# Optimization experiments

Hardware: AMD Instinct MI355X
Metric: run time of the kernel (lower is better)

The kernel has to match this reference:

```python
import jax, jax.numpy as jnp
import numpy as np

B, C_IN, C_MID, C_OUT, H, W = 256, 2, 128, 64, 15, 15
N_RES = 4  # line_length//2 - 1 with line_length=11

# per-direction input offsets for kernel taps w0 and w2 (w1 is always center),
# matching fix_direction_order=True sparse 3x3 kernel construction:
# dir0 horizontal, dir1 vertical, dir2 anti-diagonal, dir3 main diagonal.
OFFSETS = (((0, -1), (0, 1)),
           ((-1, 0), (1, 0)),
           ((1, -1), (-1, 1)),
           ((-1, -1), (1, 1)))


def shift2d(x, di, dj):
    # out[..., i, j] = x[..., i+di, j+dj] with zero padding (di,dj in {-1,0,1})
    nd = x.ndim
    xp = jnp.pad(x, [(0, 0)] * (nd - 2) + [(1, 1), (1, 1)])
    h, w = x.shape[-2], x.shape[-1]
    return xp[..., 1 + di:1 + di + h, 1 + dj:1 + dj + w]


def dir_conv(x, w, b):
    # x: [4,B,Cin,H,W]; w: [Cout,Cin,3]; b: [Cout]
    x0 = jnp.stack([shift2d(x[d], *OFFSETS[d][0]) for d in range(4)])
    x2 = jnp.stack([shift2d(x[d], *OFFSETS[d][1]) for d in range(4)])
    y = (jnp.einsum('oc,dbchw->dbohw', w[..., 0], x0)
         + jnp.einsum('oc,dbchw->dbohw', w[..., 1], x)
         + jnp.einsum('oc,dbchw->dbohw', w[..., 2], x2))
    return y + b[None, None, :, None, None]


def conv1x1(x, w, b):
    # x: [4,B,Cin,H,W]; w: [Cout,Cin]; b: [Cout]
    return jnp.einsum('oc,dbchw->dbohw', w, x) + b[None, None, :, None, None]


def setup_inputs() -> dict:
    key = jax.random.key(0)
    ks = jax.random.split(key, 16)
    s_in = 1.0 / np.sqrt(3 * C_IN)
    s_mid = 1.0 / np.sqrt(3 * C_MID)
    s_pw = 1.0 / np.sqrt(C_MID)
    return {
        'x': jax.random.normal(ks[0], (B, C_IN, H, W), jnp.float32),
        'dconv0_w': jax.random.normal(ks[1], (C_MID, C_IN, 3), jnp.float32) * s_in,
        'dconv0_b': jnp.zeros((C_MID,), jnp.float32),
        'res_dconv_w': jax.random.normal(ks[2], (N_RES, C_MID, C_MID, 3), jnp.float32) * s_mid,
        'res_dconv_b': jnp.zeros((N_RES, C_MID), jnp.float32),
        'res_pw_w': jax.random.normal(ks[3], (N_RES, C_MID, C_MID), jnp.float32) * s_pw,
        'res_pw_b': jnp.zeros((N_RES, C_MID), jnp.float32),
        'c0_w1': jax.random.normal(ks[4], (C_MID, C_MID), jnp.float32) * s_pw,
        'c0_b1': jnp.zeros((C_MID,), jnp.float32),
        'c0_w2': jax.random.normal(ks[5], (C_MID, C_MID), jnp.float32) * s_pw,
        'c0_b2': jnp.zeros((C_MID,), jnp.float32),
        'final_w': jax.random.normal(ks[6], (C_OUT, C_MID), jnp.float32) * s_pw,
        'final_b': jnp.zeros((C_OUT,), jnp.float32),
    }


def reference(x, dconv0_w, dconv0_b, res_dconv_w, res_dconv_b,
              res_pw_w, res_pw_b, c0_w1, c0_b1, c0_w2, c0_b2,
              final_w, final_b):
    act = jax.nn.silu
    # all 4 direction streams start from the same input plane
    h = jnp.broadcast_to(x[None], (4,) + x.shape)  # [4,B,Cin,H,W]
    h = act(dir_conv(h, dconv0_w, dconv0_b))
    # DirectionalConvResBlocks (norm='none')
    for i in range(N_RES):
        r = h
        h = act(dir_conv(h, res_dconv_w[i], res_dconv_b[i]))
        h = act(conv1x1(h, res_pw_w[i], res_pw_b[i]))
        h = h + r
    # Conv0dResBlock (two 1x1 convs, middle_dim_multipler=1)
    r = h
    h = act(conv1x1(h, c0_w1, c0_b1))
    h = act(conv1x1(h, c0_w2, c0_b2))
    h = h + r
    # final 1x1 conv, then stack directions at dim=1 -> [B,4,Cout,H,W]
    h = conv1x1(h, final_w, final_b)
    return jnp.transpose(h, (1, 0, 2, 3, 4))
```

## Files before the change

kernel.cpp:

```cpp
#include <hip/hip_runtime.h>

using u16 = unsigned short;
using u32 = unsigned int;

typedef __bf16 bf16x8 __attribute__((ext_vector_type(8)));
typedef float  f32x4  __attribute__((ext_vector_type(4)));

#define NPOS   225
#define NT     15
#define ROWP   136
#define A_ROWS 289
#define B_ROWS 241
#define A_ELEMS (A_ROWS*ROWP)
#define B_ELEMS (B_ROWS*ROWP)
#define LDS_BYTES ((A_ELEMS + B_ELEMS)*2)
#define RSTRIDE17 (17*ROWP)

#define WA_PER_L 49152
#define WP_OFF   (4*WA_PER_L)
#define WP_PER   16384
#define WF_OFF   (WP_OFF + 6*WP_PER)
#define W_U16_TOTAL (WF_OFF + 8192)

__device__ __forceinline__ float bflo(u32 q){ return __uint_as_float(q << 16); }
__device__ __forceinline__ float bfhi(u32 q){ return __uint_as_float(q & 0xffff0000u); }
__device__ __forceinline__ u16 f2bf(float f){
  u32 u = __float_as_uint(f);
  return (u16)((u + 0x7fffu + ((u >> 16) & 1u)) >> 16);
}
__device__ __forceinline__ u32 packbf(float a, float b){
  union { __bf16 h[2]; u32 u; } r;
  r.h[0] = (__bf16)a; r.h[1] = (__bf16)b;
  return r.u;
}
__device__ __forceinline__ float silu_f(float x){
  return x * __builtin_amdgcn_rcpf(1.f + __expf(-x));
}
__device__ __forceinline__ f32x4 mfma16(bf16x8 a, bf16x8 b, f32x4 c){
  return __builtin_amdgcn_mfma_f32_16x16x32_bf16(a, b, c, 0, 0, 0);
}

__global__ void prep_w(const float* __restrict__ d0w, const float* __restrict__ rdw,
                       const float* __restrict__ rpw, const float* __restrict__ c1w,
                       const float* __restrict__ c2w, const float* __restrict__ fw,
                       float* __restrict__ ws)
{
  u16* wsb = (u16*)(ws + 768);
  const int total = 768 + W_U16_TOTAL;
  for (int idx = blockIdx.x*blockDim.x + threadIdx.x; idx < total; idx += gridDim.x*blockDim.x){
    if (idx < 768){
      int k = idx >> 7, o = idx & 127;
      ws[idx] = d0w[o*6 + k];
      continue;
    }
    int e = idx - 768;
    float v;
    if (e < WP_OFF){
      int L = e / WA_PER_L, r = e % WA_PER_L;
      int w = r / 6144, r2 = r % 6144;
      int t = r2 >> 11, r3 = r2 & 2047;
      int kb = r3 >> 9, r4 = r3 & 511;
      int l = r4 >> 3, j = r4 & 7;
      int o = w*16 + (l & 15);
      int c = kb*32 + ((l >> 4) << 3) + j;
      v = rdw[((L*128 + o)*128 + c)*3 + t];
    } else if (e < WF_OFF){
      int t2 = e - WP_OFF;
      int i = t2 / WP_PER, r = t2 % WP_PER;
      int w = r >> 11, r2 = r & 2047;
      int kb = r2 >> 9, r3 = r2 & 511;
      int l = r3 >> 3, j = r3 & 7;
      int o = w*16 + (l & 15);
      int c = kb*32 + ((l >> 4) << 3) + j;
      v = (i < 4) ? rpw[(i*128 + o)*128 + c]
        : (i == 4) ? c1w[o*128 + c] : c2w[o*128 + c];
    } else {
      int e2 = e - WF_OFF;
      int ot = e2 >> 11, r = e2 & 2047;
      int kb = r >> 9, r2 = r & 511;
      int l = r2 >> 3, j = r2 & 7;
      int o = ot*16 + (l & 15);
      int c = kb*32 + ((l >> 4) << 3) + j;
      v = fw[o*128 + c];
    }
    wsb[e] = f2bf(v);
  }
}

__device__ __forceinline__ void dconv_mfma(const u16* __restrict__ As, u16* __restrict__ Bs,
    const u16* __restrict__ wloc, const float* __restrict__ bias,
    int lane, int ot, int T0, int T1, int off0, int off2)
{
  const int col = lane & 15, kg = lane >> 4, koff = kg*8;
  bf16x8 wa[12];
  #pragma unroll
  for (int f=0; f<12; ++f)
    wa[f] = *(const bf16x8*)(wloc + ot*6144 + f*512 + lane*8);
  f32x4 bz = *(const f32x4*)(bias + ot*16 + kg*4);
  const int c1 = (col+1)*ROWP;
  #pragma unroll 1
  for (int tile=T0; tile<T1; ++tile){
    int rb = (tile+1)*RSTRIDE17 + c1;
    const u16* s0 = As + rb + off0 + koff;
    const u16* s1 = As + rb + koff;
    const u16* s2 = As + rb + off2 + koff;
    f32x4 a0 = bz;
    __builtin_amdgcn_s_setprio(1);
    #pragma unroll
    for (int kb=0; kb<4; ++kb){
      bf16x8 v0 = *(const bf16x8*)(s0 + kb*32);
      bf16x8 v1 = *(const bf16x8*)(s1 + kb*32);
      bf16x8 v2 = *(const bf16x8*)(s2 + kb*32);
      a0 = mfma16(wa[kb],   v0, a0);
      a0 = mfma16(wa[4+kb], v1, a0);
      a0 = mfma16(wa[8+kb], v2, a0);
    }
    __builtin_amdgcn_s_setprio(0);
    if (col < 15){
      u16* dp = Bs + (tile*16+col)*ROWP + ot*16 + kg*4;
      uint2 w0; w0.x = packbf(silu_f(a0[0]), silu_f(a0[1]));
      w0.y = packbf(silu_f(a0[2]), silu_f(a0[3]));
      *(uint2*)dp = w0;
    }
  }
}

template<bool SRC_HALO, bool DST_HALO, bool RESID>
__device__ __forceinline__ void pw_mfma(const u16* __restrict__ src, u16* __restrict__ dst,
    const u16* __restrict__ wloc, const float* __restrict__ bias,
    int lane, int og2, int T0, int T1)
{
  const int col = lane & 15, kg = lane >> 4, koff = kg*8;
  bf16x8 wp[2][4];
  #pragma unroll
  for (int ot=0; ot<2; ++ot)
    #pragma unroll
    for (int kb=0; kb<4; ++kb)
      wp[ot][kb] = *(const bf16x8*)(wloc + (og2*2+ot)*2048 + kb*512 + lane*8);
  f32x4 bz0 = *(const f32x4*)(bias + og2*32 + kg*4);
  f32x4 bz1 = *(const f32x4*)(bias + og2*32 + 16 + kg*4);
  const int chb = og2*32 + kg*4;
  const int c1 = (col+1)*ROWP;
  #pragma unroll 2
  for (int tile=T0; tile<T1; ++tile){
    int r1 = (tile+1)*17 + col + 1;
    int p2 = tile*16 + col;
    int rsrc = SRC_HALO ? r1*ROWP : p2*ROWP;
    const u16* S = src + rsrc + koff;
    f32x4 a0 = bz0, a1 = bz1;
    __builtin_amdgcn_s_setprio(1);
    #pragma unroll
    for (int kb=0; kb<4; ++kb){
      bf16x8 v = *(const bf16x8*)(S + kb*32);
      a0 = mfma16(wp[0][kb], v, a0);
      a1 = mfma16(wp[1][kb], v, a1);
    }
    __builtin_amdgcn_s_setprio(0);
    if (col < 15){
      int rdst = DST_HALO ? r1*ROWP : p2*ROWP;
      u16* dp = dst + rdst + chb;
      float s0 = silu_f(a0[0]), s1 = silu_f(a0[1]), s2 = silu_f(a0[2]), s3 = silu_f(a0[3]);
      float t0 = silu_f(a1[0]), t1 = silu_f(a1[1]), t2 = silu_f(a1[2]), t3 = silu_f(a1[3]);
      if (RESID){
        uint2 r0 = *(const uint2*)dp;
        uint2 r1v = *(const uint2*)(dp+16);
        s0 += bflo(r0.x); s1 += bfhi(r0.x); s2 += bflo(r0.y); s3 += bfhi(r0.y);
        t0 += bflo(r1v.x); t1 += bfhi(r1v.x); t2 += bflo(r1v.y); t3 += bfhi(r1v.y);
      }
      uint2 w0; w0.x = packbf(s0, s1); w0.y = packbf(s2, s3);
      *(uint2*)dp = w0;
      uint2 w1; w1.x = packbf(t0, t1); w1.y = packbf(t2, t3);
      *(uint2*)(dp+16) = w1;
    }
  }
}

__global__ void __launch_bounds__(1024, 1)
mix9_main(const float* __restrict__ x,
          const float* __restrict__ b_d0,
          const float* __restrict__ b_rd,
          const float* __restrict__ b_rp,
          const float* __restrict__ b_c1,
          const float* __restrict__ b_c2,
          const float* __restrict__ b_fin,
          const float* __restrict__ wt,
          float* __restrict__ out)
{
  extern __shared__ u16 sm[];
  u16* As = sm;
  u16* Bs = sm + A_ELEMS;

  const int blk  = blockIdx.x;
  const int b    = blk >> 2, d = blk & 3;
  const int tid  = threadIdx.x;
  const int wave = __builtin_amdgcn_readfirstlane(tid >> 6);
  const int lane = tid & 63;

  const int ogd  = wave >> 1;
  const int phd  = wave & 1;
  const int T0d  = phd * 8;
  const int T1d  = phd ? NT : 8;
  const int og2  = wave >> 2;
  const int ph4  = wave & 3;
  const int T0p  = ph4 * 4;
  const int T1p  = (ph4 == 3) ? NT : T0p + 4;
  const int ob   = (wave & 7) * 16;
  const int phal = wave >> 3;

  const int DI0[4] = {0,-1, 1,-1}, DJ0[4] = {-1, 0,-1,-1};
  const int DI2[4] = {0, 1,-1, 1}, DJ2[4] = { 1, 0, 1, 1};
  const int di0 = DI0[d], dj0 = DJ0[d], di2 = DI2[d], dj2 = DJ2[d];
  const int off0 = (di0*17 + dj0)*ROWP;
  const int off2 = (di2*17 + dj2)*ROWP;

  for (int k2 = tid; k2 < A_ELEMS; k2 += 1024) As[k2] = 0;
  float* xs = (float*)Bs;
  for (int k2 = tid; k2 < 2*NPOS; k2 += 1024) xs[k2] = x[b*(2*NPOS) + k2];
  __syncthreads();

  #pragma unroll 1
  for (int pb = 0; pb < 2; ++pb){
    int pp = phal*128 + pb*64 + lane;
    int i = pp >> 4, j = pp & 15;
    if (i >= 15 || j >= 15) continue;
    float acc[16];
    #pragma unroll
    for (int oo=0;oo<16;++oo) acc[oo] = b_d0[ob+oo];
    #pragma unroll
    for (int c=0;c<2;++c){
      int i0=i+di0, j0=j+dj0, i2=i+di2, j2=j+dj2;
      float x0 = ((unsigned)i0<15u && (unsigned)j0<15u) ? xs[c*NPOS + i0*15 + j0] : 0.f;
      float x1 = xs[c*NPOS + i*15 + j];
      float x2 = ((unsigned)i2<15u && (unsigned)j2<15u) ? xs[c*NPOS + i2*15 + j2] : 0.f;
      const float* w0r = wt + (c*3+0)*128 + ob;
      const float* w1r = wt + (c*3+1)*128 + ob;
      const float* w2r = wt + (c*3+2)*128 + ob;
      #pragma unroll
      for (int oo=0;oo<16;++oo)
        acc[oo] = fmaf(w0r[oo],x0, fmaf(w1r[oo],x1, fmaf(w2r[oo],x2, acc[oo])));
    }
    u16* dp = As + ((i+1)*17 + (j+1))*ROWP + ob;
    #pragma unroll
    for (int oo=0;oo<16;oo+=2)
      *(u32*)(dp+oo) = packbf(silu_f(acc[oo]), silu_f(acc[oo+1]));
  }
  __syncthreads();

  const u16* wsb = (const u16*)(wt + 768);

  #pragma unroll 1
  for (int L = 0; L < 4; ++L){
    dconv_mfma(As, Bs, wsb + L*WA_PER_L, b_rd + L*128, lane, ogd, T0d, T1d, off0, off2);
    __syncthreads();
    pw_mfma<false,true,true>(Bs, As, wsb + WP_OFF + L*WP_PER, b_rp + L*128, lane, og2, T0p, T1p);
    __syncthreads();
  }

  pw_mfma<true,false,false>(As, Bs, wsb + WP_OFF + 4*WP_PER, b_c1, lane, og2, T0p, T1p);
  __syncthreads();
  pw_mfma<false,true,true>(Bs, As, wsb + WP_OFF + 5*WP_PER, b_c2, lane, og2, T0p, T1p);
  __syncthreads();

  {
    const int col = lane & 15, kg = lane >> 4, koff = kg*8;
    const int ogf = wave >> 2;
    const int phf = wave & 3;
    const int T0f = phf * 4;
    const int T1f = (phf == 3) ? NT : T0f + 4;
    const u16* wl = wsb + WF_OFF + ogf*2048;
    bf16x8 wf[4];
    #pragma unroll
    for (int kb=0;kb<4;++kb) wf[kb] = *(const bf16x8*)(wl + (kb*64 + lane)*8);
    f32x4 bias4 = *(const f32x4*)(b_fin + ogf*16 + kg*4);
    const int c1 = (col+1)*ROWP;
    #pragma unroll 1
    for (int tile = T0f; tile < T1f; ++tile){
      int rb = (tile+1)*RSTRIDE17 + c1;
      const u16* S = As + rb + koff;
      f32x4 acc = bias4;
      #pragma unroll
      for (int kb=0;kb<4;++kb)
        acc = mfma16(wf[kb], *(const bf16x8*)(S + kb*32), acc);
      if (col < 15){
        float* op = out + ((size_t)((b*4 + d)*64 + ogf*16 + kg*4))*NPOS + tile*15 + col;
        op[0]      = acc[0];
        op[NPOS]   = acc[1];
        op[2*NPOS] = acc[2];
        op[3*NPOS] = acc[3];
      }
    }
  }
}

extern "C" void kernel_launch(void* const* d_in, const int* in_sizes, int n_in,
                              void* d_out, int out_size, void* d_ws, size_t ws_size,
                              hipStream_t stream)
{
  const float* x     = (const float*)d_in[0];
  const float* w_d0  = (const float*)d_in[1];
  const float* b_d0  = (const float*)d_in[2];
  const float* w_rd  = (const float*)d_in[3];
  const float* b_rd  = (const float*)d_in[4];
  const float* w_rp  = (const float*)d_in[5];
  const float* b_rp  = (const float*)d_in[6];
  const float* w_c1  = (const float*)d_in[7];
  const float* b_c1  = (const float*)d_in[8];
  const float* w_c2  = (const float*)d_in[9];
  const float* b_c2  = (const float*)d_in[10];
  const float* w_fin = (const float*)d_in[11];
  const float* b_fin = (const float*)d_in[12];
  float* wt  = (float*)d_ws;
  float* out = (float*)d_out;

  prep_w<<<128, 512, 0, stream>>>(w_d0, w_rd, w_rp, w_c1, w_c2, w_fin, wt);

  (void)hipFuncSetAttribute((const void*)mix9_main,
                            hipFuncAttributeMaxDynamicSharedMemorySize, LDS_BYTES);
  mix9_main<<<1024, 1024, LDS_BYTES, stream>>>(x, b_d0, b_rd, b_rp, b_c1, b_c2, b_fin, wt, out);
}
```

Baseline: 244.3 us.

## Widen per-wave output tiles so each LDS activation load feeds more MFMAs

The 16 waves are re-partitioned so each wave computes more output-channel groups over fewer spatial tiles. In the directional conv, each wave now computes two 16-channel groups across up to four tiles with fully unrolled register accumulators, loading weights per tap. In the pointwise and final convs, each wave computes four or two channel groups over one or two tiles. Each LDS activation fragment is now reused by 2-4 MFMAs instead of 1-2, cutting LDS read traffic, at the cost of higher register pressure and an uneven split where the last wave group gets fewer tiles.

```diff
diff --git a/kernel.cpp b/kernel.cpp
--- a/kernel.cpp
+++ b/kernel.cpp
@@ -87,90 +87,145 @@
   }
 }
 
+template<int NTL>
 __device__ __forceinline__ void dconv_mfma(const u16* __restrict__ As, u16* __restrict__ Bs,
     const u16* __restrict__ wloc, const float* __restrict__ bias,
-    int lane, int ot, int T0, int T1, int off0, int off2)
+    int lane, int og, int T0, int off0, int off2)
 {
   const int col = lane & 15, kg = lane >> 4, koff = kg*8;
-  bf16x8 wa[12];
-  #pragma unroll
-  for (int f=0; f<12; ++f)
-    wa[f] = *(const bf16x8*)(wloc + ot*6144 + f*512 + lane*8);
-  f32x4 bz = *(const f32x4*)(bias + ot*16 + kg*4);
-  const int c1 = (col+1)*ROWP;
-  #pragma unroll 1
-  for (int tile=T0; tile<T1; ++tile){
-    int rb = (tile+1)*RSTRIDE17 + c1;
-    const u16* s0 = As + rb + off0 + koff;
-    const u16* s1 = As + rb + koff;
-    const u16* s2 = As + rb + off2 + koff;
-    f32x4 a0 = bz;
-    __builtin_amdgcn_s_setprio(1);
-    #pragma unroll
-    for (int kb=0; kb<4; ++kb){
-      bf16x8 v0 = *(const bf16x8*)(s0 + kb*32);
-      bf16x8 v1 = *(const bf16x8*)(s1 + kb*32);
-      bf16x8 v2 = *(const bf16x8*)(s2 + kb*32);
-      a0 = mfma16(wa[kb],   v0, a0);
-      a0 = mfma16(wa[4+kb], v1, a0);
-      a0 = mfma16(wa[8+kb], v2, a0);
-    }
-    __builtin_amdgcn_s_setprio(0);
-    if (col < 15){
-      u16* dp = Bs + (tile*16+col)*ROWP + ot*16 + kg*4;
-      uint2 w0; w0.x = packbf(silu_f(a0[0]), silu_f(a0[1]));
-      w0.y = packbf(silu_f(a0[2]), silu_f(a0[3]));
-      *(uint2*)dp = w0;
-    }
-  }
-}
-
-template<bool SRC_HALO, bool DST_HALO, bool RESID>
+  f32x4 bz0 = *(const f32x4*)(bias + og*32 + kg*4);
+  f32x4 bz1 = *(const f32x4*)(bias + og*32 + 16 + kg*4);
+  f32x4 acc0[NTL], acc1[NTL];
+  #pragma unroll
+  for (int t=0;t<NTL;++t){ acc0[t]=bz0; acc1[t]=bz1; }
+  const int c1 = (col+1)*ROWP + koff;
+  #pragma unroll
+  for (int tap=0; tap<3; ++tap){
+    const int offr = (tap==0) ? off0 : (tap==1) ? 0 : off2;
+    bf16x8 w0[4], w1[4];
+    #pragma unroll
+    for (int kb=0;kb<4;++kb){
+      w0[kb] = *(const bf16x8*)(wloc + (2*og  )*6144 + (tap*4+kb)*512 + lane*8);
+      w1[kb] = *(const bf16x8*)(wloc + (2*og+1)*6144 + (tap*4+kb)*512 + lane*8);
+    }
+    #pragma unroll
+    for (int t=0;t<NTL;++t){
+      const u16* s = As + (T0+t+1)*RSTRIDE17 + c1 + offr;
+      __builtin_amdgcn_s_setprio(1);
+      #pragma unroll
+      for (int kb=0;kb<4;++kb){
+        bf16x8 v = *(const bf16x8*)(s + kb*32);
+        acc0[t] = mfma16(w0[kb], v, acc0[t]);
+        acc1[t] = mfma16(w1[kb], v, acc1[t]);
+      }
+      __builtin_amdgcn_s_setprio(0);
+    }
+  }
+  if (col < 15){
+    #pragma unroll
+    for (int t=0;t<NTL;++t){
+      u16* dp = Bs + ((T0+t)*16+col)*ROWP + og*32 + kg*4;
+      uint2 v0; v0.x = packbf(silu_f(acc0[t][0]), silu_f(acc0[t][1]));
+      v0.y = packbf(silu_f(acc0[t][2]), silu_f(acc0[t][3]));
+      *(uint2*)dp = v0;
+      uint2 v1; v1.x = packbf(silu_f(acc1[t][0]), silu_f(acc1[t][1]));
+      v1.y = packbf(silu_f(acc1[t][2]), silu_f(acc1[t][3]));
+      *(uint2*)(dp+16) = v1;
+    }
+  }
+}
+
+template<int NTL, bool SRC_HALO, bool DST_HALO, bool RESID>
 __device__ __forceinline__ void pw_mfma(const u16* __restrict__ src, u16* __restrict__ dst,
     const u16* __restrict__ wloc, const float* __restrict__ bias,
-    int lane, int og2, int T0, int T1)
+    int lane, int og2, int T0)
 {
   const int col = lane & 15, kg = lane >> 4, koff = kg*8;
-  bf16x8 wp[2][4];
-  #pragma unroll
-  for (int ot=0; ot<2; ++ot)
+  bf16x8 wp[4][4];
+  #pragma unroll
+  for (int ot=0; ot<4; ++ot)
     #pragma unroll
     for (int kb=0; kb<4; ++kb)
-      wp[ot][kb] = *(const bf16x8*)(wloc + (og2*2+ot)*2048 + kb*512 + lane*8);
-  f32x4 bz0 = *(const f32x4*)(bias + og2*32 + kg*4);
-  f32x4 bz1 = *(const f32x4*)(bias + og2*32 + 16 + kg*4);
-  const int chb = og2*32 + kg*4;
-  const int c1 = (col+1)*ROWP;
-  #pragma unroll 2
-  for (int tile=T0; tile<T1; ++tile){
-    int r1 = (tile+1)*17 + col + 1;
-    int p2 = tile*16 + col;
-    int rsrc = SRC_HALO ? r1*ROWP : p2*ROWP;
-    const u16* S = src + rsrc + koff;
-    f32x4 a0 = bz0, a1 = bz1;
+      wp[ot][kb] = *(const bf16x8*)(wloc + (og2*4+ot)*2048 + kb*512 + lane*8);
+  f32x4 bz[4];
+  #pragma unroll
+  for (int ot=0; ot<4; ++ot) bz[ot] = *(const f32x4*)(bias + og2*64 + ot*16 + kg*4);
+  const int c1 = (col+1)*ROWP + koff;
+  #pragma unroll
+  for (int t=0;t<NTL;++t){
+    const int tile = T0 + t;
+    const int rh = (tile+1)*RSTRIDE17 + c1;
+    const int rc = (tile*16+col)*ROWP + koff;
+    const u16* S = src + (SRC_HALO ? rh : rc);
+    f32x4 a0 = bz[0], a1 = bz[1], a2 = bz[2], a3 = bz[3];
     __builtin_amdgcn_s_setprio(1);
     #pragma unroll
     for (int kb=0; kb<4; ++kb){
       bf16x8 v = *(const bf16x8*)(S + kb*32);
       a0 = mfma16(wp[0][kb], v, a0);
       a1 = mfma16(wp[1][kb], v, a1);
+      a2 = mfma16(wp[2][kb], v, a2);
+      a3 = mfma16(wp[3][kb], v, a3);
     }
     __builtin_amdgcn_s_setprio(0);
     if (col < 15){
-      int rdst = DST_HALO ? r1*ROWP : p2*ROWP;
-      u16* dp = dst + rdst + chb;
-      float s0 = silu_f(a0[0]), s1 = silu_f(a0[1]), s2 = silu_f(a0[2]), s3 = silu_f(a0[3]);
-      float t0 = silu_f(a1[0]), t1 = silu_f(a1[1]), t2 = silu_f(a1[2]), t3 = silu_f(a1[3]);
-      if (RESID){
-        uint2 r0 = *(const uint2*)dp;
-        uint2 r1v = *(const uint2*)(dp+16);
-        s0 += bflo(r0.x); s1 += bfhi(r0.x); s2 += bflo(r0.y); s3 += bfhi(r0.y);
-        t0 += bflo(r1v.x); t1 += bfhi(r1v.x); t2 += bflo(r1v.y); t3 += bfhi(r1v.y);
+      u16* dp = dst + (DST_HALO ? rh : rc) - koff + og2*64 + kg*4;
+      f32x4 aa[4] = {a0, a1, a2, a3};
+      #pragma unroll
+      for (int ot=0; ot<4; ++ot){
+        u16* dq = dp + ot*16;
+        float s0 = silu_f(aa[ot][0]), s1 = silu_f(aa[ot][1]);
+        float s2 = silu_f(aa[ot][2]), s3 = silu_f(aa[ot][3]);
+        if (RESID){
+          uint2 r = *(const uint2*)dq;
+          s0 += bflo(r.x); s1 += bfhi(r.x); s2 += bflo(r.y); s3 += bfhi(r.y);
+        }
+        uint2 w0v; w0v.x = packbf(s0, s1); w0v.y = packbf(s2, s3);
+        *(uint2*)dq = w0v;
       }
-      uint2 w0; w0.x = packbf(s0, s1); w0.y = packbf(s2, s3);
-      *(uint2*)dp = w0;
-      uint2 w1; w1.x = packbf(t0, t1); w1.y = packbf(t2, t3);
-      *(uint2*)(dp+16) = w1;
+    }
+  }
+}
+
+template<int NTL>
+__device__ __forceinline__ void fin_mfma(const u16* __restrict__ As,
+    const u16* __restrict__ wloc, const float* __restrict__ bias,
+    float* __restrict__ out, int lane, int ogf, int T0, int bd)
+{
+  const int col = lane & 15, kg = lane >> 4, koff = kg*8;
+  bf16x8 wf[2][4];
+  #pragma unroll
+  for (int ot=0; ot<2; ++ot)
+    #pragma unroll
+    for (int kb=0; kb<4; ++kb)
+      wf[ot][kb] = *(const bf16x8*)(wloc + (ogf*2+ot)*2048 + kb*512 + lane*8);
+  f32x4 bz0 = *(const f32x4*)(bias + ogf*32 + kg*4);
+  f32x4 bz1 = *(const f32x4*)(bias + ogf*32 + 16 + kg*4);
+  const int c1 = (col+1)*ROWP + koff;
+  #pragma unroll
+  for (int t=0;t<NTL;++t){
+    const int tile = T0 + t;
+    const u16* S = As + (tile+1)*RSTRIDE17 + c1;
+    f32x4 a0 = bz0, a1 = bz1;
+    __builtin_amdgcn_s_setprio(1);
+    #pragma unroll
+    for (int kb=0; kb<4; ++kb){
+      bf16x8 v = *(const bf16x8*)(S + kb*32);
+      a0 = mfma16(wf[0][kb], v, a0);
+      a1 = mfma16(wf[1][kb], v, a1);
+    }
+    __builtin_amdgcn_s_setprio(0);
+    if (col < 15){
+      float* op = out + ((size_t)(bd*64 + ogf*32 + kg*4))*NPOS + tile*15 + col;
+      op[0]      = a0[0];
+      op[NPOS]   = a0[1];
+      op[2*NPOS] = a0[2];
+      op[3*NPOS] = a0[3];
+      float* oq = op + 16*NPOS;
+      oq[0]      = a1[0];
+      oq[NPOS]   = a1[1];
+      oq[2*NPOS] = a1[2];
+      oq[3*NPOS] = a1[3];
     }
   }
 }
@@ -196,14 +251,10 @@
   const int wave = __builtin_amdgcn_readfirstlane(tid >> 6);
   const int lane = tid & 63;
 
-  const int ogd  = wave >> 1;
-  const int phd  = wave & 1;
-  const int T0d  = phd * 8;
-  const int T1d  = phd ? NT : 8;
-  const int og2  = wave >> 2;
-  const int ph4  = wave & 3;
-  const int T0p  = ph4 * 4;
-  const int T1p  = (ph4 == 3) ? NT : T0p + 4;
+  const int ogd  = wave >> 2;
+  const int pgd  = wave & 3;
+  const int og2  = wave >> 3;
+  const int pg8  = wave & 7;
   const int ob   = (wave & 7) * 16;
   const int phal = wave >> 3;
 
@@ -250,46 +301,33 @@
 
   #pragma unroll 1
   for (int L = 0; L < 4; ++L){
-    dconv_mfma(As, Bs, wsb + L*WA_PER_L, b_rd + L*128, lane, ogd, T0d, T1d, off0, off2);
+    if (pgd == 3)
+      dconv_mfma<3>(As, Bs, wsb + L*WA_PER_L, b_rd + L*128, lane, ogd, 12, off0, off2);
+    else
+      dconv_mfma<4>(As, Bs, wsb + L*WA_PER_L, b_rd + L*128, lane, ogd, pgd*4, off0, off2);
     __syncthreads();
-    pw_mfma<false,true,true>(Bs, As, wsb + WP_OFF + L*WP_PER, b_rp + L*128, lane, og2, T0p, T1p);
+    if (pg8 == 7)
+      pw_mfma<1,false,true,true>(Bs, As, wsb + WP_OFF + L*WP_PER, b_rp + L*128, lane, og2, 14);
+    else
+      pw_mfma<2,false,true,true>(Bs, As, wsb + WP_OFF + L*WP_PER, b_rp + L*128, lane, og2, pg8*2);
     __syncthreads();
   }
 
-  pw_mfma<true,false,false>(As, Bs, wsb + WP_OFF + 4*WP_PER, b_c1, lane, og2, T0p, T1p);
+  if (pg8 == 7)
+    pw_mfma<1,true,false,false>(As, Bs, wsb + WP_OFF + 4*WP_PER, b_c1, lane, og2, 14);
+  else
+    pw_mfma<2,true,false,false>(As, Bs, wsb + WP_OFF + 4*WP_PER, b_c1, lane, og2, pg8*2);
   __syncthreads();
-  pw_mfma<false,true,true>(Bs, As, wsb + WP_OFF + 5*WP_PER, b_c2, lane, og2, T0p, T1p);
+  if (pg8 == 7)
+    pw_mfma<1,false,true,true>(Bs, As, wsb + WP_OFF + 5*WP_PER, b_c2, lane, og2, 14);
+  else
+    pw_mfma<2,false,true,true>(Bs, As, wsb + WP_OFF + 5*WP_PER, b_c2, lane, og2, pg8*2);
   __syncthreads();
 
-  {
-    const int col = lane & 15, kg = lane >> 4, koff = kg*8;
-    const int ogf = wave >> 2;
-    const int phf = wave & 3;
-    const int T0f = phf * 4;
-    const int T1f = (phf == 3) ? NT : T0f + 4;
-    const u16* wl = wsb + WF_OFF + ogf*2048;
-    bf16x8 wf[4];
-    #pragma unroll
-    for (int kb=0;kb<4;++kb) wf[kb] = *(const bf16x8*)(wl + (kb*64 + lane)*8);
-    f32x4 bias4 = *(const f32x4*)(b_fin + ogf*16 + kg*4);
-    const int c1 = (col+1)*ROWP;
-    #pragma unroll 1
-    for (int tile = T0f; tile < T1f; ++tile){
-      int rb = (tile+1)*RSTRIDE17 + c1;
-      const u16* S = As + rb + koff;
-      f32x4 acc = bias4;
-      #pragma unroll
-      for (int kb=0;kb<4;++kb)
-        acc = mfma16(wf[kb], *(const bf16x8*)(S + kb*32), acc);
-      if (col < 15){
-        float* op = out + ((size_t)((b*4 + d)*64 + ogf*16 + kg*4))*NPOS + tile*15 + col;
-        op[0]      = acc[0];
-        op[NPOS]   = acc[1];
-        op[2*NPOS] = acc[2];
-        op[3*NPOS] = acc[3];
-      }
-    }
-  }
+  if (pg8 == 7)
+    fin_mfma<1>(As, wsb + WF_OFF, b_fin, out, lane, og2, 14, b*4 + d);
+  else
+    fin_mfma<2>(As, wsb + WF_OFF, b_fin, out, lane, og2, pg8*2, b*4 + d);
 }
 
 extern "C" void kernel_launch(void* const* d_in, const int* in_sizes, int n_in,
```

New measurement: 416.5 us. 70.5% more time.
